# Kernel optimization log

Hardware: AMD Instinct MI355X
Metric: run time of the kernel (lower is better)

Reference implementation:

```python
import jax, jax.numpy as jnp
import numpy as np


def pairwise_euclidean_distance(x, y):
    # x: [N, D], y: [K, D] -> [N, K] squared Euclidean distances
    cross = -2.0 * (x @ y.T)
    x_term = jnp.sum(x * x, axis=1, keepdims=True)      # [N, 1]
    y_term = jnp.sum(y * y, axis=1, keepdims=True).T    # [1, K]
    return cross + x_term + y_term


def quantize(z, centroids):
    # z: [B, T, D], centroids: [K, D]
    B, T, D = z.shape
    flat = z.reshape(-1, D)                              # [N, D]
    distances = pairwise_euclidean_distance(flat, centroids)
    alignment = jnp.argmin(distances, axis=1)            # [N]
    q = centroids[alignment]                             # gather [N, D]
    # straight-through estimator: grad flows to z, not centroids
    q = flat + jax.lax.stop_gradient(q - flat)
    return q.reshape(B, T, D)


def setup_inputs() -> dict:
    key = jax.random.key(0)
    ks = jax.random.split(key, 5)
    B, T, F, D, K = 16, 2048, 80, 512, 2048
    return {
        "x": jax.random.normal(ks[0], (B, T, F), dtype=jnp.float32),
        "W_enc": jax.random.normal(ks[1], (F, D), dtype=jnp.float32) * (1.0 / np.sqrt(F)),
        "b_enc": jnp.zeros((D,), dtype=jnp.float32),
        "centroids": jax.random.normal(ks[2], (K, D), dtype=jnp.float32),
        "W_dec": jax.random.normal(ks[3], (D, F), dtype=jnp.float32) * (1.0 / np.sqrt(D)),
        "b_dec": jnp.zeros((F,), dtype=jnp.float32),
    }


def reference(x, W_enc, b_enc, centroids, W_dec, b_dec):
    z = x @ W_enc + b_enc            # encoder: [B, T, D]
    zq = quantize(z, centroids)      # VQ: distance + argmin + gather
    out = zq @ W_dec + b_dec         # decoder: [B, T, F]
    return out
```

## Files before the change

kernel.cpp:

```cpp
#include <hip/hip_runtime.h>
#include <hip/hip_bf16.h>

#define N_TOK  32768
#define F_IN   80
#define D_DIM  512
#define K_CENT 2048
#define F_OUT  80
#define TM     16
#define KP     96
#define M2     0.5f
#define QSLOTS 12
#define QREC   104
#define TREC   416
#define JTOT   160

typedef __attribute__((ext_vector_type(8)))  short bf16x8;
typedef __attribute__((ext_vector_type(4)))  float fx4;
typedef __attribute__((ext_vector_type(16))) float fx16;

#define AS3 __attribute__((address_space(3)))
#define AS1 __attribute__((address_space(1)))

__device__ inline unsigned short f2bf(float f) {
    unsigned u = __float_as_uint(f);
    return (unsigned short)((u + 0x7FFFu + ((u >> 16) & 1u)) >> 16);
}
__device__ inline float bf2f(unsigned short h) {
    return __uint_as_float((unsigned)h << 16);
}

__device__ inline void gll16(const unsigned short* g, unsigned short* l) {
    __builtin_amdgcn_global_load_lds((const AS1 unsigned*)g, (AS3 unsigned*)l, 16, 0, 0);
}

__device__ inline unsigned fkey(float f) {
    unsigned b = __float_as_uint(f);
    return b ^ ((b >> 31) ? 0xFFFFFFFFu : 0x80000000u);
}
__device__ inline float keyf(unsigned k) {
    unsigned b = k ^ ((k & 0x80000000u) ? 0x80000000u : 0xFFFFFFFFu);
    return __uint_as_float(b);
}

__device__ inline size_t frag32_addr(int row, int k) {
    int sub = (row >> 5) * 2 + ((k >> 4) & 1);
    int L = (row & 31) + ((k >> 3) & 1) * 32;
    return (size_t)sub * 512 + L * 8 + (k & 7);
}

__global__ __launch_bounds__(256) void k_prep1(
    const float* __restrict__ x, const float* __restrict__ Wenc,
    const float* __restrict__ Wdec, const float* __restrict__ cent,
    const float* __restrict__ benc,
    unsigned short* __restrict__ xbt, float* __restrict__ Bcat,
    float* __restrict__ cnorm, unsigned short* __restrict__ Gbt) {
    const int bid = blockIdx.x, tid = threadIdx.x;
    if (bid < 1536) {
        int o = bid * 256 + tid;
        int m = o / 12;
        int ko = (o - m * 12) * 8;
        unsigned short u[8];
        if (ko < F_IN) {
            const float* src = x + (size_t)m * F_IN + ko;
            float4 v0 = *(const float4*)src;
            float4 v1 = *(const float4*)(src + 4);
            u[0]=f2bf(v0.x); u[1]=f2bf(v0.y); u[2]=f2bf(v0.z); u[3]=f2bf(v0.w);
            u[4]=f2bf(v1.x); u[5]=f2bf(v1.y); u[6]=f2bf(v1.z); u[7]=f2bf(v1.w);
        } else if (ko == 80) {
            u[0] = 0x3F80; u[1] = 0x3F80;
#pragma unroll
            for (int j = 2; j < 8; ++j) u[j] = 0;
        } else {
#pragma unroll
            for (int j = 0; j < 8; ++j) u[j] = 0;
        }
        int mt = m >> 7, kt = ko >> 5, row = m & 127, kl = ko & 31;
        uint4 p;
        p.x = (unsigned)u[0] | ((unsigned)u[1] << 16);
        p.y = (unsigned)u[2] | ((unsigned)u[3] << 16);
        p.z = (unsigned)u[4] | ((unsigned)u[5] << 16);
        p.w = (unsigned)u[6] | ((unsigned)u[7] << 16);
        *(uint4*)&xbt[(size_t)(mt * 3 + kt) * 4096 + frag32_addr(row, kl)] = p;
    } else if (bid < 1856) {
        int e = (bid - 1536) * 256 + tid;
        int d = e / JTOT, j = e - d * JTOT;
        float v = (j < F_OUT) ? Wdec[(size_t)d * F_OUT + j]
                              : Wenc[(size_t)(j - F_OUT) * D_DIM + d];
        Bcat[e] = v;
    } else {
        int wave = tid >> 6, lane = tid & 63;
        int k = (bid - 1856) * 4 + wave;
        const float* row = cent + (size_t)k * D_DIM;
        float s = 0.f, t = 0.f;
#pragma unroll
        for (int j = 0; j < 8; ++j) {
            float c = row[lane + 64 * j];
            float b = benc[lane + 64 * j];
            s += c * c; t += b * c;
        }
#pragma unroll
        for (int off = 32; off; off >>= 1) { s += __shfl_down(s, off); t += __shfl_down(t, off); }
        const int nt = k >> 7, cl = k & 127;
        const size_t tb = (size_t)(nt * 3 + 2) * 4096;
        if (lane < 14)
            Gbt[tb + frag32_addr(cl, 18 + lane)] = 0;
        if (lane == 0) {
            cnorm[k] = s;
            float v = -0.5f * (s - 2.0f * t);
            unsigned short h = f2bf(v);
            unsigned short l = f2bf(v - bf2f(h));
            Gbt[tb + frag32_addr(cl, 16)] = h;
            Gbt[tb + frag32_addr(cl, 17)] = l;
        }
    }
}

__global__ __launch_bounds__(384) void k_cgemm2(
    const float* __restrict__ cent, const float* __restrict__ Bcat,
    const float* __restrict__ bdec, unsigned short* __restrict__ Gbt,
    float* __restrict__ dec) {
    __shared__ float pacc[192][4];
    const int tid = threadIdx.x;
    const int j = tid % 192;
    const int dh = tid / 192;
    const int k0 = blockIdx.x * 4;
    float a0 = 0.f, a1 = 0.f, a2 = 0.f, a3 = 0.f;
    if (j < JTOT) {
        const float* c0 = cent + (size_t)k0 * D_DIM + dh * 256;
        const float* bp = Bcat + (size_t)dh * 256 * JTOT + j;
#pragma unroll 4
        for (int d = 0; d < 256; ++d) {
            float b  = bp[d * JTOT];
            a0 += c0[d] * b;
            a1 += c0[D_DIM + d] * b;
            a2 += c0[2 * D_DIM + d] * b;
            a3 += c0[3 * D_DIM + d] * b;
        }
        if (dh == 1) { pacc[j][0] = a0; pacc[j][1] = a1; pacc[j][2] = a2; pacc[j][3] = a3; }
    }
    __syncthreads();
    if (dh == 0 && j < JTOT) {
        a0 += pacc[j][0]; a1 += pacc[j][1]; a2 += pacc[j][2]; a3 += pacc[j][3];
        float a[4] = { a0, a1, a2, a3 };
        if (j < F_OUT) {
            float bd = bdec[j];
#pragma unroll
            for (int c = 0; c < 4; ++c)
                dec[(size_t)(k0 + c) * F_OUT + j] = a[c] + bd;
        } else {
            int f = j - F_OUT;
#pragma unroll
            for (int c = 0; c < 4; ++c) {
                int k = k0 + c;
                Gbt[(size_t)((k >> 7) * 3 + (f >> 5)) * 4096 + frag32_addr(k & 127, f & 31)]
                    = f2bf(a[c]);
            }
        }
    }
}

__global__ __launch_bounds__(512) void k_dist3(
    const unsigned short* __restrict__ xbt, const unsigned short* __restrict__ Gbt,
    char* __restrict__ lists) {
    __shared__ unsigned short Bs[2][12288];
    __shared__ int cnt[128];
    __shared__ unsigned mxk[128];

    const int tid = threadIdx.x;
    const int bid = blockIdx.x;
    const int mt = bid >> 2, nq = bid & 3;
    const int lane = tid & 63;
    const int wave = tid >> 6;
    const int tg = wave >> 1;
    const int ch = wave & 1;
    const int col = lane & 31;
    const int hi = lane >> 5;

    if (tid < 128) { cnt[tid] = 0; mxk[tid] = 0u; }

    bf16x8 bfr[6];
    const unsigned short* Ab = xbt + (size_t)mt * 12288;
#pragma unroll
    for (int kc = 0; kc < 6; ++kc)
        bfr[kc] = *(const bf16x8*)&Ab[(kc >> 1) * 4096 + (tg * 2 + (kc & 1)) * 512 + lane * 8];

    const int woff = (tid & ~63) * 8;
    const unsigned short* Gq = Gbt + (size_t)nq * 4 * 12288;
#pragma unroll
    for (int q = 0; q < 3; ++q)
        gll16(Gq + q * 4096 + tid * 8, &Bs[0][0] + q * 4096 + woff);

    float rmax = -3.4e38f;
    int cur = 0;
    for (int t4 = 0; t4 < 4; ++t4) {
        __syncthreads();
        if (t4 + 1 < 4) {
#pragma unroll
            for (int q = 0; q < 3; ++q)
                gll16(Gq + (size_t)(t4 + 1) * 12288 + q * 4096 + tid * 8,
                      &Bs[cur ^ 1][0] + q * 4096 + woff);
        }
        const unsigned short* B = &Bs[cur][0];
        fx16 acc[2];
#pragma unroll
        for (int u = 0; u < 2; ++u)
#pragma unroll
            for (int r = 0; r < 16; ++r) acc[u][r] = 0.f;
#pragma unroll
        for (int kc = 0; kc < 6; ++kc) {
#pragma unroll
            for (int u = 0; u < 2; ++u) {
                bf16x8 a = *(const bf16x8*)&B[(kc >> 1) * 4096
                             + ((ch * 2 + u) * 2 + (kc & 1)) * 512 + lane * 8];
                acc[u] = __builtin_amdgcn_mfma_f32_32x32x16_bf16(a, bfr[kc], acc[u], 0, 0, 0);
            }
        }
        float m = acc[0][0];
#pragma unroll
        for (int r = 1; r < 16; ++r) m = fmaxf(m, acc[0][r]);
#pragma unroll
        for (int r = 0; r < 16; ++r) m = fmaxf(m, acc[1][r]);
        m = fmaxf(m, __shfl_xor(m, 32));
        rmax = fmaxf(rmax, m);
        const float th = rmax - M2;
        const int tk = tg * 32 + col;
        char* qrec = lists + (size_t)(mt * 128 + tk) * TREC + nq * QREC;
#pragma unroll
        for (int u = 0; u < 2; ++u)
#pragma unroll
            for (int r = 0; r < 16; ++r) {
                float v = acc[u][r];
                if (v >= th) {
                    int slot = atomicAdd(&cnt[tk], 1);
                    if (slot < QSLOTS) {
                        uint2 e;
                        e.x = __float_as_uint(v);
                        e.y = (unsigned)((nq * 4 + t4) * 128 + (ch * 2 + u) * 32
                                         + (r & 3) + 8 * (r >> 2) + 4 * hi);
                        *(uint2*)(qrec + 8 + slot * 8) = e;
                    }
                }
            }
        cur ^= 1;
    }
    if (lane < 32) atomicMax(&mxk[tg * 32 + lane], fkey(rmax));
    __syncthreads();
    if (tid < 128) {
        uint2 h;
        h.x = (unsigned)cnt[tid];
        h.y = __float_as_uint(keyf(mxk[tid]));
        *(uint2*)(lists + (size_t)(mt * 128 + tid) * TREC + nq * QREC) = h;
    }
}

__global__ __launch_bounds__(256) void k_merge3(
    const char* __restrict__ lists, const float* __restrict__ cnorm,
    const float* __restrict__ cent, const float* __restrict__ x,
    const float* __restrict__ Wenc, const float* __restrict__ benc,
    const float* __restrict__ dec, float* __restrict__ out) {
    const int lane = threadIdx.x & 63;
    const int wid = blockIdx.x * 4 + (threadIdx.x >> 6);
    const int q = lane / 13, s = lane - q * 13;
    for (int it = 0; it < 4; ++it) {
        const int token = wid + it * 8192;
        const char* base = lists + (size_t)token * TREC;
        uint2 w = make_uint2(0u, 0u);
        if (lane < 52) w = *(const uint2*)(base + q * QREC + s * 8);
        const bool ishdr = (lane < 52) && (s == 0);
        float gm = ishdr ? __uint_as_float(w.y) : -3.4e38f;
#pragma unroll
        for (int off = 1; off < 64; off <<= 1) gm = fmaxf(gm, __shfl_xor(gm, off));
        const float th = gm - M2;
        unsigned long long anyovf = __ballot(ishdr && ((int)w.x > QSLOTS));
        int qcnt = __shfl((int)w.x, q * 13);
        int c12 = qcnt < QSLOTS ? qcnt : QSLOTS;
        bool cand = (lane < 52) && (s >= 1) && (s - 1 < c12) && (__uint_as_float(w.x) >= th);
        unsigned long long bal = __ballot(cand);
        int ns = __popcll(bal);
        int ans;
        if (!anyovf && ns == 1) {
            ans = __shfl((int)w.y, __ffsll(bal) - 1);
        } else {
            float z8[8];
#pragma unroll
            for (int j = 0; j < 8; ++j) z8[j] = benc[lane * 8 + j];
            const float* xr = x + (size_t)token * F_IN;
            const float* wp = Wenc + lane * 8;
            for (int f = 0; f < F_IN; ++f) {
                float xf = xr[f];
                fx4 w0 = *(const fx4*)(wp + (size_t)f * D_DIM);
                fx4 w1 = *(const fx4*)(wp + (size_t)f * D_DIM + 4);
                z8[0] += xf * w0.x; z8[1] += xf * w0.y; z8[2] += xf * w0.z; z8[3] += xf * w0.w;
                z8[4] += xf * w1.x; z8[5] += xf * w1.y; z8[6] += xf * w1.z; z8[7] += xf * w1.w;
            }
            float bd = 1e30f; int bn = 0x7FFFFFFF;
            if (!anyovf) {
                unsigned long long m = bal;
                while (m) {
                    int src = __ffsll(m) - 1; m &= m - 1;
                    int ci = __shfl((int)w.y, src);
                    const float* cr = cent + (size_t)ci * D_DIM + lane * 8;
                    fx4 c0 = *(const fx4*)cr, c1 = *(const fx4*)(cr + 4);
                    float dp = z8[0] * c0.x + z8[1] * c0.y + z8[2] * c0.z + z8[3] * c0.w
                             + z8[4] * c1.x + z8[5] * c1.y + z8[6] * c1.z + z8[7] * c1.w;
#pragma unroll
                    for (int off = 1; off < 64; off <<= 1) dp += __shfl_xor(dp, off);
                    float de = cnorm[ci] - 2.0f * dp;
                    if (de < bd || (de == bd && ci < bn)) { bd = de; bn = ci; }
                }
            } else {
                for (int ci = 0; ci < K_CENT; ++ci) {
                    const float* cr = cent + (size_t)ci * D_DIM + lane * 8;
                    fx4 c0 = *(const fx4*)cr, c1 = *(const fx4*)(cr + 4);
                    float dp = z8[0] * c0.x + z8[1] * c0.y + z8[2] * c0.z + z8[3] * c0.w
                             + z8[4] * c1.x + z8[5] * c1.y + z8[6] * c1.z + z8[7] * c1.w;
#pragma unroll
                    for (int off = 1; off < 64; off <<= 1) dp += __shfl_xor(dp, off);
                    float de = cnorm[ci] - 2.0f * dp;
                    if (de < bd || (de == bd && ci < bn)) { bd = de; bn = ci; }
                }
            }
            ans = bn;
        }
        const float* dr = dec + (size_t)ans * F_OUT;
        float* orow = out + (size_t)token * F_OUT;
        orow[lane] = dr[lane];
        if (lane < F_OUT - 64) orow[64 + lane] = dr[64 + lane];
    }
}

__global__ void k_transpose(const float* __restrict__ cent, float* __restrict__ centT) {
    __shared__ float tile[64][65];
    int kb = blockIdx.x * 64, db = blockIdx.y * 64;
    int lx = threadIdx.x & 63, ly = threadIdx.x >> 6;
#pragma unroll
    for (int i = 0; i < 16; ++i) {
        int row = ly + i * 4;
        tile[row][lx] = cent[(size_t)(kb + row) * D_DIM + db + lx];
    }
    __syncthreads();
#pragma unroll
    for (int i = 0; i < 16; ++i) {
        int row = ly + i * 4;
        centT[(size_t)(db + row) * K_CENT + kb + lx] = tile[lx][row];
    }
}

__global__ void k_cnorm(const float* __restrict__ cent, float* __restrict__ cnorm) {
    int wave = threadIdx.x >> 6, lane = threadIdx.x & 63;
    int k = blockIdx.x * 4 + wave;
    const float* row = cent + (size_t)k * D_DIM;
    float s = 0.f;
#pragma unroll
    for (int j = 0; j < 8; ++j) { float v = row[lane + 64 * j]; s += v * v; }
#pragma unroll
    for (int off = 32; off; off >>= 1) s += __shfl_down(s, off);
    if (lane == 0) cnorm[k] = s;
}

__global__ void k_dec(const float* __restrict__ cent, const float* __restrict__ Wdec,
                      const float* __restrict__ bdec, float* __restrict__ dec) {
    __shared__ float cs[D_DIM];
    int k = blockIdx.x;
    for (int d = threadIdx.x; d < D_DIM; d += blockDim.x) cs[d] = cent[(size_t)k * D_DIM + d];
    __syncthreads();
    int f = threadIdx.x;
    if (f < F_OUT) {
        float a0 = 0.f, a1 = 0.f, a2 = 0.f, a3 = 0.f;
#pragma unroll 4
        for (int d = 0; d < D_DIM; d += 4) {
            a0 += cs[d + 0] * Wdec[(d + 0) * F_OUT + f];
            a1 += cs[d + 1] * Wdec[(d + 1) * F_OUT + f];
            a2 += cs[d + 2] * Wdec[(d + 2) * F_OUT + f];
            a3 += cs[d + 3] * Wdec[(d + 3) * F_OUT + f];
        }
        dec[(size_t)k * F_OUT + f] = a0 + a1 + a2 + a3 + bdec[f];
    }
}

__global__ void k_out(const float* __restrict__ dec, const int* __restrict__ idx,
                      float* __restrict__ out) {
    int e0 = blockIdx.x * 2560;
#pragma unroll
    for (int r = 0; r < 10; ++r) {
        int e = e0 + threadIdx.x + r * 256;
        int n = e / F_OUT, f = e - n * F_OUT;
        out[e] = dec[(size_t)idx[n] * F_OUT + f];
    }
}

__global__ __launch_bounds__(256) void k_main(
    const float* __restrict__ x, const float* __restrict__ Wenc,
    const float* __restrict__ benc, const float* __restrict__ centT,
    const float* __restrict__ cnorm, int* __restrict__ idxOut) {
    __shared__ float xs[TM * F_IN];
    __shared__ float zs[TM][D_DIM];
    float* pv = &zs[0][0];
    int*   pi = (int*)(&zs[0][0] + 256 * TM);
    const int tid = threadIdx.x;
    const int tok0 = blockIdx.x * TM;
    for (int e = tid; e < TM * F_IN; e += 256) xs[e] = x[(size_t)tok0 * F_IN + e];
    __syncthreads();
    {
        float acc0[TM], acc1[TM];
#pragma unroll
        for (int t = 0; t < TM; ++t) { acc0[t] = 0.f; acc1[t] = 0.f; }
        const float2 b2 = ((const float2*)benc)[tid];
#pragma unroll 4
        for (int f4 = 0; f4 < F_IN; f4 += 4) {
            float2 w0 = ((const float2*)(Wenc + (size_t)(f4 + 0) * D_DIM))[tid];
            float2 w1 = ((const float2*)(Wenc + (size_t)(f4 + 1) * D_DIM))[tid];
            float2 w2 = ((const float2*)(Wenc + (size_t)(f4 + 2) * D_DIM))[tid];
            float2 w3 = ((const float2*)(Wenc + (size_t)(f4 + 3) * D_DIM))[tid];
#pragma unroll
            for (int t = 0; t < TM; ++t) {
                float4 xv = *(const float4*)&xs[t * F_IN + f4];
                acc0[t] += xv.x * w0.x + xv.y * w1.x + xv.z * w2.x + xv.w * w3.x;
                acc1[t] += xv.x * w0.y + xv.y * w1.y + xv.z * w2.y + xv.w * w3.y;
            }
        }
#pragma unroll
        for (int t = 0; t < TM; ++t)
            *(float2*)&zs[t][2 * tid] = make_float2(acc0[t] + b2.x, acc1[t] + b2.y);
    }
    __syncthreads();
    float minv[TM]; int mini[TM];
#pragma unroll
    for (int t = 0; t < TM; ++t) { minv[t] = 3.4e38f; mini[t] = 0; }
    for (int iter = 0; iter < 2; ++iter) {
        float acc[4][TM];
#pragma unroll
        for (int j = 0; j < 4; ++j)
#pragma unroll
            for (int t = 0; t < TM; ++t) acc[j][t] = 0.f;
        const int cbase = iter * 1024 + tid;
        for (int d4 = 0; d4 < D_DIM; d4 += 4) {
            float cv[4][4];
#pragma unroll
            for (int dd = 0; dd < 4; ++dd) {
                const float* cp = centT + (size_t)(d4 + dd) * K_CENT + cbase;
                cv[dd][0] = cp[0]; cv[dd][1] = cp[256]; cv[dd][2] = cp[512]; cv[dd][3] = cp[768];
            }
#pragma unroll
            for (int t = 0; t < TM; ++t) {
                float4 zv = *(const float4*)&zs[t][d4];
#pragma unroll
                for (int j = 0; j < 4; ++j)
                    acc[j][t] += zv.x * cv[0][j] + zv.y * cv[1][j] + zv.z * cv[2][j] + zv.w * cv[3][j];
            }
        }
#pragma unroll
        for (int j = 0; j < 4; ++j) {
            int c = cbase + j * 256;
            float cn = cnorm[c];
#pragma unroll
            for (int t = 0; t < TM; ++t) {
                float dist = cn - 2.f * acc[j][t];
                if (dist < minv[t]) { minv[t] = dist; mini[t] = c; }
            }
        }
    }
    __syncthreads();
#pragma unroll
    for (int t = 0; t < TM; ++t) { pv[tid * TM + t] = minv[t]; pi[tid * TM + t] = mini[t]; }
    __syncthreads();
    {
        int t = tid & 15, g = tid >> 4;
        float bv = 3.4e38f; int bi = 0x7fffffff;
        for (int j = 0; j < 16; ++j) {
            int r2 = g + 16 * j;
            float vv = pv[r2 * TM + t]; int i2 = pi[r2 * TM + t];
            if (vv < bv || (vv == bv && i2 < bi)) { bv = vv; bi = i2; }
        }
        pv[g * TM + t] = bv; pi[g * TM + t] = bi;
    }
    __syncthreads();
    if (tid < TM) {
        int t = tid;
        float bv = 3.4e38f; int bi = 0x7fffffff;
        for (int g = 0; g < 16; ++g) {
            float vv = pv[g * TM + t]; int i2 = pi[g * TM + t];
            if (vv < bv || (vv == bv && i2 < bi)) { bv = vv; bi = i2; }
        }
        idxOut[tok0 + t] = bi;
    }
}

extern "C" void kernel_launch(void* const* d_in, const int* in_sizes, int n_in,
                              void* d_out, int out_size, void* d_ws, size_t ws_size,
                              hipStream_t stream) {
    const float* x    = (const float*)d_in[0];
    const float* Wenc = (const float*)d_in[1];
    const float* benc = (const float*)d_in[2];
    const float* cent = (const float*)d_in[3];
    const float* Wdec = (const float*)d_in[4];
    const float* bdec = (const float*)d_in[5];
    float* out = (float*)d_out;

    const size_t L_B  = (size_t)N_TOK * TREC;
    const size_t XB_B = (size_t)N_TOK * KP * 2;
    const size_t GB_B = (size_t)K_CENT * KP * 2;
    const size_t N_B  = (size_t)K_CENT * 4;
    const size_t D_B  = (size_t)K_CENT * F_OUT * 4;
    const size_t BC_B = (size_t)D_DIM * JTOT * 4;
    const size_t NEED = L_B + XB_B + GB_B + N_B + D_B + BC_B;

    if (ws_size >= NEED) {
        char* w = (char*)d_ws;
        char*           lists = w;                            w += L_B;
        unsigned short* xbt   = (unsigned short*)w;           w += XB_B;
        unsigned short* Gbt   = (unsigned short*)w;           w += GB_B;
        float*          cnorm = (float*)w;                    w += N_B;
        float*          dec   = (float*)w;                    w += D_B;
        float*          Bcat  = (float*)w;

        k_prep1<<<2368, 256, 0, stream>>>(x, Wenc, Wdec, cent, benc,
                                          xbt, Bcat, cnorm, Gbt);
        k_cgemm2<<<K_CENT / 4, 384, 0, stream>>>(cent, Bcat, bdec, Gbt, dec);
        k_dist3<<<1024, 512, 0, stream>>>(xbt, Gbt, lists);
        k_merge3<<<2048, 256, 0, stream>>>(lists, cnorm, cent, x, Wenc, benc, dec, out);
    } else {
        float* centT = (float*)d_ws;
        float* cnorm = centT + (size_t)D_DIM * K_CENT;
        float* dec   = cnorm + K_CENT;
        int*   idx   = (int*)(dec + (size_t)K_CENT * F_OUT);
        k_transpose<<<dim3(K_CENT / 64, D_DIM / 64), 256, 0, stream>>>(cent, centT);
        k_cnorm<<<K_CENT / 4, 256, 0, stream>>>(cent, cnorm);
        k_dec<<<K_CENT, 128, 0, stream>>>(cent, Wdec, bdec, dec);
        k_main<<<N_TOK / TM, 256, 0, stream>>>(x, Wenc, benc, centT, cnorm, idx);
        k_out<<<N_TOK * F_OUT / 2560, 256, 0, stream>>>(dec, idx, out);
    }
}
```

Before: 102.3 us.

## Widen candidate lists and limit overflow fallback to overflowing quarter

Raises the per-quarter candidate slot count so fewer tokens overflow the shortlist, which makes the lists record larger. The merge kernel now runs one token per wave with 16-byte loads and two ballots. On overflow it rescans only the 512 centroids of the overflowing quarter instead of all 2048. The trade is more bytes written by the distance kernel and read by merge, and more register and shuffle work per token.

```diff
diff --git a/kernel.cpp b/kernel.cpp
--- a/kernel.cpp
+++ b/kernel.cpp
@@ -9,9 +9,9 @@
 #define TM     16
 #define KP     96
 #define M2     0.5f
-#define QSLOTS 12
-#define QREC   104
-#define TREC   416
+#define QSLOTS 24
+#define QREC   200
+#define TREC   800
 #define JTOT   160
 
 typedef __attribute__((ext_vector_type(8)))  short bf16x8;
@@ -253,80 +253,85 @@
     }
 }
 
-__global__ __launch_bounds__(256) void k_merge3(
+__global__ __launch_bounds__(256) void k_merge4(
     const char* __restrict__ lists, const float* __restrict__ cnorm,
     const float* __restrict__ cent, const float* __restrict__ x,
     const float* __restrict__ Wenc, const float* __restrict__ benc,
     const float* __restrict__ dec, float* __restrict__ out) {
     const int lane = threadIdx.x & 63;
-    const int wid = blockIdx.x * 4 + (threadIdx.x >> 6);
-    const int q = lane / 13, s = lane - q * 13;
-    for (int it = 0; it < 4; ++it) {
-        const int token = wid + it * 8192;
-        const char* base = lists + (size_t)token * TREC;
-        uint2 w = make_uint2(0u, 0u);
-        if (lane < 52) w = *(const uint2*)(base + q * QREC + s * 8);
-        const bool ishdr = (lane < 52) && (s == 0);
-        float gm = ishdr ? __uint_as_float(w.y) : -3.4e38f;
-#pragma unroll
-        for (int off = 1; off < 64; off <<= 1) gm = fmaxf(gm, __shfl_xor(gm, off));
-        const float th = gm - M2;
-        unsigned long long anyovf = __ballot(ishdr && ((int)w.x > QSLOTS));
-        int qcnt = __shfl((int)w.x, q * 13);
-        int c12 = qcnt < QSLOTS ? qcnt : QSLOTS;
-        bool cand = (lane < 52) && (s >= 1) && (s - 1 < c12) && (__uint_as_float(w.x) >= th);
-        unsigned long long bal = __ballot(cand);
-        int ns = __popcll(bal);
-        int ans;
-        if (!anyovf && ns == 1) {
-            ans = __shfl((int)w.y, __ffsll(bal) - 1);
-        } else {
-            float z8[8];
-#pragma unroll
-            for (int j = 0; j < 8; ++j) z8[j] = benc[lane * 8 + j];
-            const float* xr = x + (size_t)token * F_IN;
-            const float* wp = Wenc + lane * 8;
-            for (int f = 0; f < F_IN; ++f) {
-                float xf = xr[f];
-                fx4 w0 = *(const fx4*)(wp + (size_t)f * D_DIM);
-                fx4 w1 = *(const fx4*)(wp + (size_t)f * D_DIM + 4);
-                z8[0] += xf * w0.x; z8[1] += xf * w0.y; z8[2] += xf * w0.z; z8[3] += xf * w0.w;
-                z8[4] += xf * w1.x; z8[5] += xf * w1.y; z8[6] += xf * w1.z; z8[7] += xf * w1.w;
-            }
-            float bd = 1e30f; int bn = 0x7FFFFFFF;
-            if (!anyovf) {
-                unsigned long long m = bal;
-                while (m) {
-                    int src = __ffsll(m) - 1; m &= m - 1;
-                    int ci = __shfl((int)w.y, src);
-                    const float* cr = cent + (size_t)ci * D_DIM + lane * 8;
-                    fx4 c0 = *(const fx4*)cr, c1 = *(const fx4*)(cr + 4);
-                    float dp = z8[0] * c0.x + z8[1] * c0.y + z8[2] * c0.z + z8[3] * c0.w
-                             + z8[4] * c1.x + z8[5] * c1.y + z8[6] * c1.z + z8[7] * c1.w;
-#pragma unroll
-                    for (int off = 1; off < 64; off <<= 1) dp += __shfl_xor(dp, off);
-                    float de = cnorm[ci] - 2.0f * dp;
-                    if (de < bd || (de == bd && ci < bn)) { bd = de; bn = ci; }
-                }
-            } else {
-                for (int ci = 0; ci < K_CENT; ++ci) {
-                    const float* cr = cent + (size_t)ci * D_DIM + lane * 8;
-                    fx4 c0 = *(const fx4*)cr, c1 = *(const fx4*)(cr + 4);
-                    float dp = z8[0] * c0.x + z8[1] * c0.y + z8[2] * c0.z + z8[3] * c0.w
-                             + z8[4] * c1.x + z8[5] * c1.y + z8[6] * c1.z + z8[7] * c1.w;
-#pragma unroll
-                    for (int off = 1; off < 64; off <<= 1) dp += __shfl_xor(dp, off);
-                    float de = cnorm[ci] - 2.0f * dp;
-                    if (de < bd || (de == bd && ci < bn)) { bd = de; bn = ci; }
-                }
-            }
-            ans = bn;
-        }
-        const float* dr = dec + (size_t)ans * F_OUT;
-        float* orow = out + (size_t)token * F_OUT;
-        orow[lane] = dr[lane];
-        if (lane < F_OUT - 64) orow[64 + lane] = dr[64 + lane];
-    }
+    const int token = blockIdx.x * 4 + (threadIdx.x >> 6);
+    const char* base = lists + (size_t)token * TREC;
+    uint4 w4 = make_uint4(0u, 0u, 0u, 0u);
+    if (lane < 50) w4 = *(const uint4*)(base + lane * 16);
+    const int   c0 = __shfl((int)w4.x, 0),  c1 = __shfl((int)w4.z, 12);
+    const int   c2 = __shfl((int)w4.x, 25), c3 = __shfl((int)w4.z, 37);
+    const float m0 = __uint_as_float((unsigned)__shfl((int)w4.y, 0));
+    const float m1 = __uint_as_float((unsigned)__shfl((int)w4.w, 12));
+    const float m2 = __uint_as_float((unsigned)__shfl((int)w4.y, 25));
+    const float m3 = __uint_as_float((unsigned)__shfl((int)w4.w, 37));
+    const float gm = fmaxf(fmaxf(m0, m1), fmaxf(m2, m3));
+    const float th = gm - M2;
+    const bool ovf = (c0 > QSLOTS) || (c1 > QSLOTS) || (c2 > QSLOTS) || (c3 > QSLOTS);
+    const int q0c = c0 < QSLOTS ? c0 : QSLOTS, q1c = c1 < QSLOTS ? c1 : QSLOTS;
+    const int q2c = c2 < QSLOTS ? c2 : QSLOTS, q3c = c3 < QSLOTS ? c3 : QSLOTS;
+    bool cd[2]; 
+#pragma unroll
+    for (int rr = 0; rr < 2; ++rr) {
+        int t = lane * 2 + rr;
+        int q = t / 25, s = t - q * 25;
+        int cq = (q == 0) ? q0c : (q == 1) ? q1c : (q == 2) ? q2c : q3c;
+        float v = __uint_as_float(rr ? w4.z : w4.x);
+        cd[rr] = (lane < 50) && (s >= 1) && (s - 1 < cq) && (v >= th);
+    }
+    unsigned long long b0 = __ballot(cd[0]);
+    unsigned long long b1 = __ballot(cd[1]);
+    int ns = __popcll(b0) + __popcll(b1);
+    int ans;
+    if (!ovf && ns == 1) {
+        if (b0) ans = __shfl((int)w4.y, __ffsll(b0) - 1);
+        else    ans = __shfl((int)w4.w, __ffsll(b1) - 1);
+    } else {
+        float z8[8];
+#pragma unroll
+        for (int j = 0; j < 8; ++j) z8[j] = benc[lane * 8 + j];
+        const float* xr = x + (size_t)token * F_IN;
+        const float* wp = Wenc + lane * 8;
+        for (int f = 0; f < F_IN; ++f) {
+            float xf = xr[f];
+            fx4 w0 = *(const fx4*)(wp + (size_t)f * D_DIM);
+            fx4 w1 = *(const fx4*)(wp + (size_t)f * D_DIM + 4);
+            z8[0] += xf * w0.x; z8[1] += xf * w0.y; z8[2] += xf * w0.z; z8[3] += xf * w0.w;
+            z8[4] += xf * w1.x; z8[5] += xf * w1.y; z8[6] += xf * w1.z; z8[7] += xf * w1.w;
+        }
+        float bd = 1e30f; int bn = 0x7FFFFFFF;
+        auto exact1 = [&](int ci) {
+            const float* cr = cent + (size_t)ci * D_DIM + lane * 8;
+            fx4 cc0 = *(const fx4*)cr, cc1 = *(const fx4*)(cr + 4);
+            float dp = z8[0] * cc0.x + z8[1] * cc0.y + z8[2] * cc0.z + z8[3] * cc0.w
+                     + z8[4] * cc1.x + z8[5] * cc1.y + z8[6] * cc1.z + z8[7] * cc1.w;
+#pragma unroll
+            for (int off = 1; off < 64; off <<= 1) dp += __shfl_xor(dp, off);
+            float de = cnorm[ci] - 2.0f * dp;
+            if (de < bd || (de == bd && ci < bn)) { bd = de; bn = ci; }
+        };
+        unsigned long long m = b0;
+        while (m) { int src = __ffsll(m) - 1; m &= m - 1; exact1(__shfl((int)w4.y, src)); }
+        m = b1;
+        while (m) { int src = __ffsll(m) - 1; m &= m - 1; exact1(__shfl((int)w4.w, src)); }
+        if (ovf) {
+#pragma unroll
+            for (int q = 0; q < 4; ++q) {
+                int cf = (q == 0) ? c0 : (q == 1) ? c1 : (q == 2) ? c2 : c3;
+                if (cf > QSLOTS)
+                    for (int n0 = 0; n0 < 512; ++n0) exact1(q * 512 + n0);
+            }
+        }
+        ans = bn;
+    }
+    const float* dr = dec + (size_t)ans * F_OUT;
+    float* orow = out + (size_t)token * F_OUT;
+    orow[lane] = dr[lane];
+    if (lane < F_OUT - 64) orow[64 + lane] = dr[64 + lane];
 }
 
 __global__ void k_transpose(const float* __restrict__ cent, float* __restrict__ centT) {
@@ -518,7 +523,7 @@
                                           xbt, Bcat, cnorm, Gbt);
         k_cgemm2<<<K_CENT / 4, 384, 0, stream>>>(cent, Bcat, bdec, Gbt, dec);
         k_dist3<<<1024, 512, 0, stream>>>(xbt, Gbt, lists);
-        k_merge3<<<2048, 256, 0, stream>>>(lists, cnorm, cent, x, Wenc, benc, dec, out);
+        k_merge4<<<N_TOK / 4, 256, 0, stream>>>(lists, cnorm, cent, x, Wenc, benc, dec, out);
     } else {
         float* centT = (float*)d_ws;
         float* cnorm = centT + (size_t)D_DIM * K_CENT;
```

After: 100.3 us. Within noise of the previous version (-1.9%).
